# Performance work log

Hardware: AMD Instinct MI355X
Metric: run time of the kernel (lower is better)

## Reference

```python
import jax, jax.numpy as jnp
import numpy as np

C = 19
IGNORE = 255
UPPER_BOUND = 1.0
SEG_W, EDGE_W, ATT_W = 1.0, 0.3, 0.1
EDGE_THRESH = 0.8


def _img_hist(t):
    # torch.histc(target, bins=C, min=0, max=C): bin i counts values in [i, i+1); 255 falls outside
    tf = t.ravel()
    inb = (tf >= 0) & (tf < C)
    idx = jnp.where(inb, tf, 0)
    return jnp.zeros((C,), jnp.float32).at[idx].add(inb.astype(jnp.float32))


def _seg_loss(segin, target):
    # per-image class-histogram weights (ImageBasedCrossEntropyLoss2d, norm=False)
    N = target.shape[0]
    bins = jax.vmap(_img_hist)(target)                      # [N, C]
    hist_norm = bins / jnp.sum(bins, axis=1, keepdims=True)
    w = (bins != 0).astype(jnp.float32) * UPPER_BOUND * (1.0 - hist_norm) + 1.0  # [N, C]

    logp = jax.nn.log_softmax(segin, axis=1)                # [N, C, H, W]
    tc = jnp.clip(target, 0, C - 1)
    lp = jnp.take_along_axis(logp, tc[:, None, :, :], axis=1)[:, 0]  # [N, H, W]
    valid = (target != IGNORE).astype(jnp.float32)
    pw = jnp.take_along_axis(w, tc.reshape(N, -1), axis=1).reshape(target.shape) * valid
    # NLLLoss(weight, reduction='mean', ignore_index): weighted mean per image, summed over batch
    num = -jnp.sum(pw * lp, axis=(1, 2))
    den = jnp.sum(pw, axis=(1, 2))
    return jnp.sum(num / den)


def _bce2d(x, t):
    # x: logits [N,1,H,W]; t: float target, 1=pos, 0=neg, >1 ignored (weight 0)
    pos = t == 1.0
    neg = t == 0.0
    pos_num = jnp.sum(pos.astype(jnp.float32))
    neg_num = jnp.sum(neg.astype(jnp.float32))
    sum_num = pos_num + neg_num
    w = jnp.where(pos, neg_num / sum_num, 0.0) + jnp.where(neg, pos_num / sum_num, 0.0)
    # stable BCE-with-logits
    bce = jnp.maximum(x, 0.0) - x * t + jnp.log1p(jnp.exp(-jnp.abs(x)))
    return jnp.mean(w * bce)


def setup_inputs() -> dict:
    key = jax.random.key(0)
    k1, k2, k3, k4 = jax.random.split(key, 4)
    N, H, W = 4, 768, 768
    segin = jax.random.normal(k1, (N, C, H, W), dtype=jnp.float32)
    edgein = jax.random.normal(k2, (N, 1, H, W), dtype=jnp.float32)
    segmask = jax.random.randint(k3, (N, H, W), 0, C, dtype=jnp.int32)
    edgemask = jax.random.randint(k4, (N, 1, H, W), 0, 2, dtype=jnp.int32)
    return {"segin": segin, "edgein": edgein, "segmask": segmask, "edgemask": edgemask}


def reference(segin, edgein, segmask, edgemask):
    seg_loss = SEG_W * _seg_loss(segin, segmask)
    edge_loss = EDGE_W * _bce2d(edgein, edgemask.astype(jnp.float32))
    # edge attention: pixels where max-channel edge logit > 0.8 keep their label, else ignore
    edge_max = jnp.max(edgein, axis=1)                      # [N, H, W]
    att_target = jnp.where(edge_max > EDGE_THRESH, segmask, IGNORE)
    att_loss = ATT_W * _seg_loss(segin, att_target)
    return seg_loss + edge_loss + att_loss
```

## Files before the change

kernel.cpp:

```cpp
#include <hip/hip_runtime.h>
#include <math.h>

#define CNUM 19
#define NB 4
#define HW 589824
#define NPIX 2359296

#define TPB 256
#define PXT 4
#define TILE (TPB * PXT)

#define HPX 8
#define HTILE (256 * HPX)

struct alignas(64) ImgAcc {
  double num_seg, den_seg, num_att, den_att, bce;
  double pad[3];
};

struct Ws {
  unsigned int hist_seg[NB][CNUM];
  unsigned int hist_att[NB][CNUM];
  unsigned int pos_num;
  unsigned int neg_num;
  ImgAcc acc[NB];
};

__global__ void k_init(Ws* ws) {
  unsigned int* p = (unsigned int*)ws;
  const int nw = (int)(sizeof(Ws) / 4);
  for (int i = threadIdx.x; i < nw; i += blockDim.x) p[i] = 0u;
}

__global__ __launch_bounds__(256, 4) void k_hist(const int* __restrict__ segmask,
                                                 const float* __restrict__ edgein,
                                                 const int* __restrict__ edgemask,
                                                 Ws* __restrict__ ws) {
  const int n   = blockIdx.y;
  const int tid = threadIdx.x;
  const int base = n * HW + blockIdx.x * HTILE + tid * 4;

  unsigned int cs[CNUM], ca[CNUM];
  #pragma unroll
  for (int c = 0; c < CNUM; ++c) { cs[c] = 0u; ca[c] = 0u; }
  unsigned int cp = 0u, cn = 0u;

  #pragma unroll 2
  for (int it = 0; it < HPX / 4; ++it) {
    const int idx = base + it * 1024;
    int4   sv = *reinterpret_cast<const int4*>(segmask + idx);
    float4 e  = *reinterpret_cast<const float4*>(edgein + idx);
    int4   mv = *reinterpret_cast<const int4*>(edgemask + idx);
    int   sa[4] = {sv.x, sv.y, sv.z, sv.w};
    float ea[4] = {e.x, e.y, e.z, e.w};
    int   ma[4] = {mv.x, mv.y, mv.z, mv.w};
    #pragma unroll
    for (int p = 0; p < 4; ++p) {
      const int s = sa[p];
      const bool inb = ((unsigned)s) < (unsigned)CNUM;
      const unsigned long long attm = __ballot(ea[p] > 0.8f);
      #pragma unroll
      for (int c = 0; c < CNUM; ++c) {
        unsigned long long bm = __ballot(inb && (s == c));
        cs[c] += (unsigned)__popcll(bm);
        ca[c] += (unsigned)__popcll(bm & attm);
      }
      cp += (unsigned)__popcll(__ballot(ma[p] == 1));
      cn += (unsigned)__popcll(__ballot(ma[p] == 0));
    }
  }

  __shared__ unsigned int red[4][2 * CNUM + 2];
  const int wave = tid >> 6;
  const int lane = tid & 63;
  if (lane == 0) {
    #pragma unroll
    for (int c = 0; c < CNUM; ++c) { red[wave][c] = cs[c]; red[wave][CNUM + c] = ca[c]; }
    red[wave][2 * CNUM] = cp;
    red[wave][2 * CNUM + 1] = cn;
  }
  __syncthreads();
  if (tid < 2 * CNUM + 2) {
    unsigned int v = red[0][tid] + red[1][tid] + red[2][tid] + red[3][tid];
    if (tid < CNUM)               atomicAdd(&ws->hist_seg[n][tid], v);
    else if (tid < 2 * CNUM)      atomicAdd(&ws->hist_att[n][tid - CNUM], v);
    else if (tid == 2 * CNUM)     atomicAdd(&ws->pos_num, v);
    else                          atomicAdd(&ws->neg_num, v);
  }
}

__global__ __launch_bounds__(TPB, 4) void k_main(const float* __restrict__ segin,
                                                 const float* __restrict__ edgein,
                                                 const int* __restrict__ segmask,
                                                 const int* __restrict__ edgemask,
                                                 const Ws* __restrict__ ws,
                                                 Ws* __restrict__ wsw) {
  const int n = blockIdx.y;
  const int t = threadIdx.x;
  const int tile0 = blockIdx.x * TILE;

  __shared__ float lws[CNUM], lwa[CNUM];
  __shared__ float redlds[TPB / 64][5];

  if (t < CNUM) {
    float total = 0.f;
    #pragma unroll
    for (int i = 0; i < CNUM; ++i) total += (float)ws->hist_seg[n][i];
    float bins = (float)ws->hist_seg[n][t];
    lws[t] = (bins != 0.f ? (1.0f - bins / total) : 0.f) + 1.0f;
  } else if (t >= 64 && t < 64 + CNUM) {
    int c = t - 64;
    float total = 0.f;
    #pragma unroll
    for (int i = 0; i < CNUM; ++i) total += (float)ws->hist_att[n][i];
    float bins = (float)ws->hist_att[n][c];
    lwa[c] = (bins != 0.f ? (1.0f - bins / total) : 0.f) + 1.0f;
  }
  const unsigned int pn = ws->pos_num, nn = ws->neg_num;
  const float inv_sum = 1.0f / (float)(pn + nn);
  const float wpos = (float)nn * inv_sum;
  const float wneg = (float)pn * inv_sum;
  __syncthreads();

  const int pxoff = n * HW + tile0 + t * 4;

  int4 tm = *reinterpret_cast<const int4*>(segmask + pxoff);
  int tcv[PXT];
  unsigned int validbits = 0u;
  {
    int ta[4] = {tm.x, tm.y, tm.z, tm.w};
    #pragma unroll
    for (int j = 0; j < 4; ++j) {
      tcv[j] = min(max(ta[j], 0), CNUM - 1);
      validbits |= (ta[j] != 255) ? (1u << j) : 0u;
    }
  }

  float sacc[PXT] = {0.f, 0.f, 0.f, 0.f};
  float xt[PXT]   = {0.f, 0.f, 0.f, 0.f};

  const float* cb = segin + (size_t)n * CNUM * HW + tile0 + t * 4;
  #pragma unroll
  for (int c = 0; c < CNUM; ++c) {
    float4 v = *reinterpret_cast<const float4*>(cb + (size_t)c * HW);
    float va[4] = {v.x, v.y, v.z, v.w};
    #pragma unroll
    for (int j = 0; j < 4; ++j) {
      sacc[j] += __expf(va[j]);
      xt[j] = (tcv[j] == c) ? va[j] : xt[j];
    }
  }

  float4 ev = *reinterpret_cast<const float4*>(edgein + pxoff);
  int4   em = *reinterpret_cast<const int4*>(edgemask + pxoff);

  float acc_num_s = 0.f, acc_den_s = 0.f, acc_num_a = 0.f, acc_den_a = 0.f, acc_bce = 0.f;
  {
    float ea[4] = {ev.x, ev.y, ev.z, ev.w};
    int   ma[4] = {em.x, em.y, em.z, em.w};
    #pragma unroll
    for (int j = 0; j < PXT; ++j) {
      float lp = xt[j] - __logf(sacc[j]);
      bool valid = (validbits >> j) & 1u;
      float pw_s = valid ? lws[tcv[j]] : 0.f;
      acc_num_s -= pw_s * lp;
      acc_den_s += pw_s;

      float e = ea[j];
      bool valida = valid && (e > 0.8f);
      float pw_a = valida ? lwa[tcv[j]] : 0.f;
      acc_num_a -= pw_a * lp;
      acc_den_a += pw_a;

      int emv = ma[j];
      float bce = fmaxf(e, 0.f) - e * (float)emv + log1pf(__expf(-fabsf(e)));
      float wb = (emv == 1) ? wpos : ((emv == 0) ? wneg : 0.f);
      acc_bce += wb * bce;
    }
  }

  #pragma unroll
  for (int off = 32; off > 0; off >>= 1) {
    acc_num_s += __shfl_down(acc_num_s, off);
    acc_den_s += __shfl_down(acc_den_s, off);
    acc_num_a += __shfl_down(acc_num_a, off);
    acc_den_a += __shfl_down(acc_den_a, off);
    acc_bce   += __shfl_down(acc_bce, off);
  }
  const int wave = t >> 6;
  const int lane = t & 63;
  if (lane == 0) {
    redlds[wave][0] = acc_num_s; redlds[wave][1] = acc_den_s;
    redlds[wave][2] = acc_num_a; redlds[wave][3] = acc_den_a;
    redlds[wave][4] = acc_bce;
  }
  __syncthreads();
  if (t == 0) {
    float r0 = redlds[0][0] + redlds[1][0] + redlds[2][0] + redlds[3][0];
    float r1 = redlds[0][1] + redlds[1][1] + redlds[2][1] + redlds[3][1];
    float r2 = redlds[0][2] + redlds[1][2] + redlds[2][2] + redlds[3][2];
    float r3 = redlds[0][3] + redlds[1][3] + redlds[2][3] + redlds[3][3];
    float r4 = redlds[0][4] + redlds[1][4] + redlds[2][4] + redlds[3][4];
    atomicAdd(&wsw->acc[n].num_seg, (double)r0);
    atomicAdd(&wsw->acc[n].den_seg, (double)r1);
    atomicAdd(&wsw->acc[n].num_att, (double)r2);
    atomicAdd(&wsw->acc[n].den_att, (double)r3);
    atomicAdd(&wsw->acc[n].bce,     (double)r4);
  }
}

__global__ void k_final(const Ws* __restrict__ ws, float* __restrict__ out) {
  if (threadIdx.x == 0 && blockIdx.x == 0) {
    double segl = 0.0, attl = 0.0, bces = 0.0;
    for (int i = 0; i < NB; ++i) {
      segl += ws->acc[i].num_seg / ws->acc[i].den_seg;
      attl += ws->acc[i].num_att / ws->acc[i].den_att;
      bces += ws->acc[i].bce;
    }
    double edgel = bces / (double)NPIX;
    out[0] = (float)(segl + 0.3 * edgel + 0.1 * attl);
  }
}

extern "C" void kernel_launch(void* const* d_in, const int* in_sizes, int n_in,
                              void* d_out, int out_size, void* d_ws, size_t ws_size,
                              hipStream_t stream) {
  const float* segin   = (const float*)d_in[0];
  const float* edgein  = (const float*)d_in[1];
  const int*   segmask = (const int*)d_in[2];
  const int*   edgemask= (const int*)d_in[3];
  Ws* ws = (Ws*)d_ws;
  float* out = (float*)d_out;

  hipLaunchKernelGGL(k_init,  dim3(1),               dim3(128), 0, stream, ws);
  hipLaunchKernelGGL(k_hist,  dim3(HW / HTILE, NB),  dim3(256), 0, stream, segmask, edgein, edgemask, ws);
  hipLaunchKernelGGL(k_main,  dim3(HW / TILE, NB),   dim3(TPB), 0, stream, segin, edgein, segmask, edgemask, ws, ws);
  hipLaunchKernelGGL(k_final, dim3(1),               dim3(1),   0, stream, ws, out);
}
```

Measured before the change: 322.4 us.

## Fuse histogram pass into main kernel via per-class loss sums

Removes the separate histogram kernel by rewriting the class-weighted NLL as per-class sums of -log p and per-class counts, which are accumulated in shared memory with atomics and combined with the weights in the final kernel. The BCE term is likewise split into positive and negative partial sums so the pos/neg weights can be applied afterwards. This saves one full read of segmask, edgein and edgemask and one kernel launch. Segin and edgein loads also become nontemporal. In exchange it adds contended per-pixel LDS float atomics and more global double atomics per block.

```diff
diff --git a/kernel.cpp b/kernel.cpp
--- a/kernel.cpp
+++ b/kernel.cpp
@@ -10,20 +10,20 @@
 #define PXT 4
 #define TILE (TPB * PXT)
 
-#define HPX 8
-#define HTILE (256 * HPX)
+typedef float f32x4 __attribute__((ext_vector_type(4)));
 
-struct alignas(64) ImgAcc {
-  double num_seg, den_seg, num_att, den_att, bce;
-  double pad[3];
+struct ImgAcc2 {
+  double sS[CNUM];
+  double sA[CNUM];
+  unsigned int cS[CNUM];
+  unsigned int cA[CNUM];
+  unsigned int pad[2];
 };
 
 struct Ws {
-  unsigned int hist_seg[NB][CNUM];
-  unsigned int hist_att[NB][CNUM];
-  unsigned int pos_num;
-  unsigned int neg_num;
-  ImgAcc acc[NB];
+  ImgAcc2 img[NB];
+  double bce_p, bce_n;
+  unsigned int np, nn;
 };
 
 __global__ void k_init(Ws* ws) {
@@ -32,107 +32,36 @@
   for (int i = threadIdx.x; i < nw; i += blockDim.x) p[i] = 0u;
 }
 
-__global__ __launch_bounds__(256, 4) void k_hist(const int* __restrict__ segmask,
-                                                 const float* __restrict__ edgein,
-                                                 const int* __restrict__ edgemask,
-                                                 Ws* __restrict__ ws) {
-  const int n   = blockIdx.y;
-  const int tid = threadIdx.x;
-  const int base = n * HW + blockIdx.x * HTILE + tid * 4;
-
-  unsigned int cs[CNUM], ca[CNUM];
-  #pragma unroll
-  for (int c = 0; c < CNUM; ++c) { cs[c] = 0u; ca[c] = 0u; }
-  unsigned int cp = 0u, cn = 0u;
-
-  #pragma unroll 2
-  for (int it = 0; it < HPX / 4; ++it) {
-    const int idx = base + it * 1024;
-    int4   sv = *reinterpret_cast<const int4*>(segmask + idx);
-    float4 e  = *reinterpret_cast<const float4*>(edgein + idx);
-    int4   mv = *reinterpret_cast<const int4*>(edgemask + idx);
-    int   sa[4] = {sv.x, sv.y, sv.z, sv.w};
-    float ea[4] = {e.x, e.y, e.z, e.w};
-    int   ma[4] = {mv.x, mv.y, mv.z, mv.w};
-    #pragma unroll
-    for (int p = 0; p < 4; ++p) {
-      const int s = sa[p];
-      const bool inb = ((unsigned)s) < (unsigned)CNUM;
-      const unsigned long long attm = __ballot(ea[p] > 0.8f);
-      #pragma unroll
-      for (int c = 0; c < CNUM; ++c) {
-        unsigned long long bm = __ballot(inb && (s == c));
-        cs[c] += (unsigned)__popcll(bm);
-        ca[c] += (unsigned)__popcll(bm & attm);
-      }
-      cp += (unsigned)__popcll(__ballot(ma[p] == 1));
-      cn += (unsigned)__popcll(__ballot(ma[p] == 0));
-    }
-  }
-
-  __shared__ unsigned int red[4][2 * CNUM + 2];
-  const int wave = tid >> 6;
-  const int lane = tid & 63;
-  if (lane == 0) {
-    #pragma unroll
-    for (int c = 0; c < CNUM; ++c) { red[wave][c] = cs[c]; red[wave][CNUM + c] = ca[c]; }
-    red[wave][2 * CNUM] = cp;
-    red[wave][2 * CNUM + 1] = cn;
-  }
-  __syncthreads();
-  if (tid < 2 * CNUM + 2) {
-    unsigned int v = red[0][tid] + red[1][tid] + red[2][tid] + red[3][tid];
-    if (tid < CNUM)               atomicAdd(&ws->hist_seg[n][tid], v);
-    else if (tid < 2 * CNUM)      atomicAdd(&ws->hist_att[n][tid - CNUM], v);
-    else if (tid == 2 * CNUM)     atomicAdd(&ws->pos_num, v);
-    else                          atomicAdd(&ws->neg_num, v);
-  }
-}
-
-__global__ __launch_bounds__(TPB, 4) void k_main(const float* __restrict__ segin,
-                                                 const float* __restrict__ edgein,
-                                                 const int* __restrict__ segmask,
-                                                 const int* __restrict__ edgemask,
-                                                 const Ws* __restrict__ ws,
-                                                 Ws* __restrict__ wsw) {
+__global__ __launch_bounds__(TPB, 4) void k_fused(const float* __restrict__ segin,
+                                                  const float* __restrict__ edgein,
+                                                  const int* __restrict__ segmask,
+                                                  const int* __restrict__ edgemask,
+                                                  Ws* __restrict__ wsw) {
   const int n = blockIdx.y;
   const int t = threadIdx.x;
   const int tile0 = blockIdx.x * TILE;
 
-  __shared__ float lws[CNUM], lwa[CNUM];
-  __shared__ float redlds[TPB / 64][5];
+  __shared__ float lsS[CNUM], lsA[CNUM];
+  __shared__ unsigned int lcS[CNUM], lcA[CNUM];
+  __shared__ float sbp, sbn;
+  __shared__ unsigned int snp, snn;
 
-  if (t < CNUM) {
-    float total = 0.f;
-    #pragma unroll
-    for (int i = 0; i < CNUM; ++i) total += (float)ws->hist_seg[n][i];
-    float bins = (float)ws->hist_seg[n][t];
-    lws[t] = (bins != 0.f ? (1.0f - bins / total) : 0.f) + 1.0f;
-  } else if (t >= 64 && t < 64 + CNUM) {
-    int c = t - 64;
-    float total = 0.f;
-    #pragma unroll
-    for (int i = 0; i < CNUM; ++i) total += (float)ws->hist_att[n][i];
-    float bins = (float)ws->hist_att[n][c];
-    lwa[c] = (bins != 0.f ? (1.0f - bins / total) : 0.f) + 1.0f;
-  }
-  const unsigned int pn = ws->pos_num, nn = ws->neg_num;
-  const float inv_sum = 1.0f / (float)(pn + nn);
-  const float wpos = (float)nn * inv_sum;
-  const float wneg = (float)pn * inv_sum;
+  if (t < CNUM) { lsS[t] = 0.f; lsA[t] = 0.f; lcS[t] = 0u; lcA[t] = 0u; }
+  if (t == CNUM)     { sbp = 0.f; sbn = 0.f; }
+  if (t == CNUM + 1) { snp = 0u;  snn = 0u; }
   __syncthreads();
 
   const int pxoff = n * HW + tile0 + t * 4;
 
   int4 tm = *reinterpret_cast<const int4*>(segmask + pxoff);
   int tcv[PXT];
-  unsigned int validbits = 0u;
+  unsigned int inbits = 0u;
   {
     int ta[4] = {tm.x, tm.y, tm.z, tm.w};
     #pragma unroll
     for (int j = 0; j < 4; ++j) {
       tcv[j] = min(max(ta[j], 0), CNUM - 1);
-      validbits |= (ta[j] != 255) ? (1u << j) : 0u;
+      inbits |= (((unsigned)ta[j]) < (unsigned)CNUM) ? (1u << j) : 0u;
     }
   }
 
@@ -142,7 +71,8 @@
   const float* cb = segin + (size_t)n * CNUM * HW + tile0 + t * 4;
   #pragma unroll
   for (int c = 0; c < CNUM; ++c) {
-    float4 v = *reinterpret_cast<const float4*>(cb + (size_t)c * HW);
+    f32x4 v = __builtin_nontemporal_load(
+        reinterpret_cast<const f32x4*>(cb + (size_t)c * HW));
     float va[4] = {v.x, v.y, v.z, v.w};
     #pragma unroll
     for (int j = 0; j < 4; ++j) {
@@ -151,73 +81,94 @@
     }
   }
 
-  float4 ev = *reinterpret_cast<const float4*>(edgein + pxoff);
+  f32x4 ev = __builtin_nontemporal_load(reinterpret_cast<const f32x4*>(edgein + pxoff));
   int4   em = *reinterpret_cast<const int4*>(edgemask + pxoff);
 
-  float acc_num_s = 0.f, acc_den_s = 0.f, acc_num_a = 0.f, acc_den_a = 0.f, acc_bce = 0.f;
+  float bpos = 0.f, bneg = 0.f;
+  int cntp = 0, cntn = 0;
   {
     float ea[4] = {ev.x, ev.y, ev.z, ev.w};
     int   ma[4] = {em.x, em.y, em.z, em.w};
     #pragma unroll
     for (int j = 0; j < PXT; ++j) {
-      float lp = xt[j] - __logf(sacc[j]);
-      bool valid = (validbits >> j) & 1u;
-      float pw_s = valid ? lws[tcv[j]] : 0.f;
-      acc_num_s -= pw_s * lp;
-      acc_den_s += pw_s;
-
+      float nlp = __logf(sacc[j]) - xt[j];
+      if ((inbits >> j) & 1u) {
+        atomicAdd(&lsS[tcv[j]], nlp);
+        atomicAdd(&lcS[tcv[j]], 1u);
+        if (ea[j] > 0.8f) {
+          atomicAdd(&lsA[tcv[j]], nlp);
+          atomicAdd(&lcA[tcv[j]], 1u);
+        }
+      }
       float e = ea[j];
-      bool valida = valid && (e > 0.8f);
-      float pw_a = valida ? lwa[tcv[j]] : 0.f;
-      acc_num_a -= pw_a * lp;
-      acc_den_a += pw_a;
-
-      int emv = ma[j];
-      float bce = fmaxf(e, 0.f) - e * (float)emv + log1pf(__expf(-fabsf(e)));
-      float wb = (emv == 1) ? wpos : ((emv == 0) ? wneg : 0.f);
-      acc_bce += wb * bce;
+      int m = ma[j];
+      float bce = fmaxf(e, 0.f) - e * (float)m + log1pf(__expf(-fabsf(e)));
+      if (m == 1) { bpos += bce; ++cntp; }
+      else if (m == 0) { bneg += bce; ++cntn; }
     }
   }
 
   #pragma unroll
   for (int off = 32; off > 0; off >>= 1) {
-    acc_num_s += __shfl_down(acc_num_s, off);
-    acc_den_s += __shfl_down(acc_den_s, off);
-    acc_num_a += __shfl_down(acc_num_a, off);
-    acc_den_a += __shfl_down(acc_den_a, off);
-    acc_bce   += __shfl_down(acc_bce, off);
+    bpos += __shfl_down(bpos, off);
+    bneg += __shfl_down(bneg, off);
+    cntp += __shfl_down(cntp, off);
+    cntn += __shfl_down(cntn, off);
   }
-  const int wave = t >> 6;
-  const int lane = t & 63;
-  if (lane == 0) {
-    redlds[wave][0] = acc_num_s; redlds[wave][1] = acc_den_s;
-    redlds[wave][2] = acc_num_a; redlds[wave][3] = acc_den_a;
-    redlds[wave][4] = acc_bce;
+  if ((t & 63) == 0) {
+    atomicAdd(&sbp, bpos);
+    atomicAdd(&sbn, bneg);
+    atomicAdd(&snp, (unsigned int)cntp);
+    atomicAdd(&snn, (unsigned int)cntn);
   }
   __syncthreads();
-  if (t == 0) {
-    float r0 = redlds[0][0] + redlds[1][0] + redlds[2][0] + redlds[3][0];
-    float r1 = redlds[0][1] + redlds[1][1] + redlds[2][1] + redlds[3][1];
-    float r2 = redlds[0][2] + redlds[1][2] + redlds[2][2] + redlds[3][2];
-    float r3 = redlds[0][3] + redlds[1][3] + redlds[2][3] + redlds[3][3];
-    float r4 = redlds[0][4] + redlds[1][4] + redlds[2][4] + redlds[3][4];
-    atomicAdd(&wsw->acc[n].num_seg, (double)r0);
-    atomicAdd(&wsw->acc[n].den_seg, (double)r1);
-    atomicAdd(&wsw->acc[n].num_att, (double)r2);
-    atomicAdd(&wsw->acc[n].den_att, (double)r3);
-    atomicAdd(&wsw->acc[n].bce,     (double)r4);
+
+  if (t < CNUM) {
+    atomicAdd(&wsw->img[n].sS[t], (double)lsS[t]);
+  } else if (t >= 32 && t < 32 + CNUM) {
+    atomicAdd(&wsw->img[n].sA[t - 32], (double)lsA[t - 32]);
+  } else if (t >= 64 && t < 64 + CNUM) {
+    unsigned int v = lcS[t - 64];
+    if (v) atomicAdd(&wsw->img[n].cS[t - 64], v);
+  } else if (t >= 96 && t < 96 + CNUM) {
+    unsigned int v = lcA[t - 96];
+    if (v) atomicAdd(&wsw->img[n].cA[t - 96], v);
+  } else if (t == 128) {
+    atomicAdd(&wsw->bce_p, (double)sbp);
+  } else if (t == 129) {
+    atomicAdd(&wsw->bce_n, (double)sbn);
+  } else if (t == 130) {
+    atomicAdd(&wsw->np, snp);
+  } else if (t == 131) {
+    atomicAdd(&wsw->nn, snn);
   }
 }
 
 __global__ void k_final(const Ws* __restrict__ ws, float* __restrict__ out) {
   if (threadIdx.x == 0 && blockIdx.x == 0) {
-    double segl = 0.0, attl = 0.0, bces = 0.0;
+    double segl = 0.0, attl = 0.0;
     for (int i = 0; i < NB; ++i) {
-      segl += ws->acc[i].num_seg / ws->acc[i].den_seg;
-      attl += ws->acc[i].num_att / ws->acc[i].den_att;
-      bces += ws->acc[i].bce;
+      const ImgAcc2* a = &ws->img[i];
+      double totS = 0.0, totA = 0.0;
+      for (int c = 0; c < CNUM; ++c) { totS += (double)a->cS[c]; totA += (double)a->cA[c]; }
+      double numS = 0.0, denS = 0.0, numA = 0.0, denA = 0.0;
+      for (int c = 0; c < CNUM; ++c) {
+        double bS = (double)a->cS[c];
+        double wS = (bS != 0.0 ? (1.0 - bS / totS) : 0.0) + 1.0;
+        numS += wS * a->sS[c];
+        denS += wS * bS;
+        double bA = (double)a->cA[c];
+        double wA = (bA != 0.0 ? (1.0 - bA / totA) : 0.0) + 1.0;
+        numA += wA * a->sA[c];
+        denA += wA * bA;
+      }
+      segl += numS / denS;
+      attl += numA / denA;
     }
-    double edgel = bces / (double)NPIX;
+    double s = (double)ws->np + (double)ws->nn;
+    double wpos = (double)ws->nn / s;
+    double wneg = (double)ws->np / s;
+    double edgel = (wpos * ws->bce_p + wneg * ws->bce_n) / (double)NPIX;
     out[0] = (float)(segl + 0.3 * edgel + 0.1 * attl);
   }
 }
@@ -232,8 +183,7 @@
   Ws* ws = (Ws*)d_ws;
   float* out = (float*)d_out;
 
-  hipLaunchKernelGGL(k_init,  dim3(1),               dim3(128), 0, stream, ws);
-  hipLaunchKernelGGL(k_hist,  dim3(HW / HTILE, NB),  dim3(256), 0, stream, segmask, edgein, edgemask, ws);
-  hipLaunchKernelGGL(k_main,  dim3(HW / TILE, NB),   dim3(TPB), 0, stream, segin, edgein, segmask, edgemask, ws, ws);
-  hipLaunchKernelGGL(k_final, dim3(1),               dim3(1),   0, stream, ws, out);
+  hipLaunchKernelGGL(k_init,  dim3(1),             dim3(256), 0, stream, ws);
+  hipLaunchKernelGGL(k_fused, dim3(HW / TILE, NB), dim3(TPB), 0, stream, segin, edgein, segmask, edgemask, ws);
+  hipLaunchKernelGGL(k_final, dim3(1),             dim3(1),   0, stream, ws, out);
 }
```

New measurement: 353.7 us. +9.7%, slower.
